# Kernel tuning notes

Hardware: AMD Instinct MI355X
Metric: run time of the kernel (lower is better)

The kernel has to match this reference:

```python
import jax, jax.numpy as jnp
import numpy as np

# Quantization constants from the original module
X_ZP = -66   # int8 zero point
Y_ZP = 160   # uint8 zero point


def setup_inputs() -> dict:
    key = jax.random.key(0)
    k1, k2 = jax.random.split(key)
    # x: [7, B, M, K] int8 in [-128, 127]
    x = jax.random.randint(k1, (7, 8, 512, 1024), -128, 128, dtype=jnp.int32).astype(jnp.int8)
    # y: [B, K, N] uint8 in [0, 255]
    y = jax.random.randint(k2, (8, 1024, 512), 0, 256, dtype=jnp.int32).astype(jnp.uint8)
    return {
        "x": x,
        "y": y,
        "x_scale": jnp.float32(0.03),
        "y_scale": jnp.float32(0.025),
    }


def reference(x, y, x_scale, y_scale):
    # dequantize_per_tensor: (q - zero_point) * scale
    xf = (x.astype(jnp.float32) - jnp.float32(X_ZP)) * x_scale   # [7, B, M, K]
    yf = (y.astype(jnp.float32) - jnp.float32(Y_ZP)) * y_scale   # [B, K, N]
    # torch.matmul broadcast: [7,B,M,K] @ [B,K,N] -> [7,B,M,N]
    return jnp.einsum('gbmk,bkn->gbmn', xf, yf)
```

## Files before the change

kernel.cpp:

```cpp
#include <hip/hip_runtime.h>
#include <stdint.h>

#define AS1 __attribute__((address_space(1)))
#define AS3 __attribute__((address_space(3)))

typedef int v4i __attribute__((ext_vector_type(4)));

constexpr int G = 7, B = 8, M = 512, N = 512, K = 1024;
constexpr int GBn = G * B;

constexpr size_t YT_BYTES = (size_t)B * N * K;
constexpr size_t CSP_CNT  = (size_t)16 * B * N;
constexpr size_t WS_NEEDED = YT_BYTES + CSP_CNT * 4;

__global__ __launch_bounds__(256) void transpose_pack_y(const int* __restrict__ y,
                                                        signed char* __restrict__ yt,
                                                        int* __restrict__ csp) {
    __shared__ unsigned char tile[64][80];
    int n0  = blockIdx.x * 64;
    int k0t = blockIdx.y;
    int k0  = k0t * 64;
    int b   = blockIdx.z;
    int t   = threadIdx.x;

    int r  = t >> 2;
    int c0 = (t & 3) * 16;
    const int* src = y + ((size_t)b * K + k0 + r) * N + n0 + c0;
    uint32_t p[4];
#pragma unroll
    for (int q = 0; q < 4; ++q) {
        int4 v = ((const int4*)src)[q];
        p[q] =  (uint32_t)((v.x & 255) ^ 128)
             | ((uint32_t)((v.y & 255) ^ 128) << 8)
             | ((uint32_t)((v.z & 255) ^ 128) << 16)
             | ((uint32_t)((v.w & 255) ^ 128) << 24);
    }
    *(uint4*)&tile[r][c0] = make_uint4(p[0], p[1], p[2], p[3]);
    __syncthreads();

    int nl = t >> 2;
    int kc = (t & 3) * 16;
    uint32_t q[4];
    int s = 0;
#pragma unroll
    for (int w = 0; w < 4; ++w) {
        uint32_t b0 = tile[kc + w * 4 + 0][nl];
        uint32_t b1 = tile[kc + w * 4 + 1][nl];
        uint32_t b2 = tile[kc + w * 4 + 2][nl];
        uint32_t b3 = tile[kc + w * 4 + 3][nl];
        s += (int)(signed char)b0 + (int)(signed char)b1
           + (int)(signed char)b2 + (int)(signed char)b3;
        q[w] = b0 | (b1 << 8) | (b2 << 16) | (b3 << 24);
    }
    *(uint4*)(yt + ((size_t)b * N + n0 + nl) * K + k0 + kc) = make_uint4(q[0], q[1], q[2], q[3]);

    s += __shfl_xor(s, 1, 64);
    s += __shfl_xor(s, 2, 64);
    if ((t & 3) == 0) csp[(size_t)k0t * (B * N) + b * N + n0 + nl] = s;
}

__global__ __launch_bounds__(512, 4) void gemm_fused(const int* __restrict__ x,
                                                     const signed char* __restrict__ yt,
                                                     const int* __restrict__ csp,
                                                     const float* __restrict__ xsp,
                                                     const float* __restrict__ ysp,
                                                     float* __restrict__ out) {
    __shared__ __align__(16) signed char As[2][128 * 64];
    __shared__ __align__(16) signed char Bs[2][256 * 64];
    __shared__ int cs_lds[256];
    __shared__ int rs_lds[128];

    int id   = blockIdx.x;
    int swz  = (id & 7) * 56 + (id >> 3);
    int gb   = swz >> 3;
    int tile = swz & 7;
    int mt   = tile >> 1;
    int nt   = tile & 1;
    int b    = gb & 7;

    int tid = threadIdx.x, wave = tid >> 6, lane = tid & 63;

    if (tid < 256) {
        int s = 0;
        const int* p = csp + b * N + nt * 256 + tid;
#pragma unroll
        for (int kt = 0; kt < 16; ++kt) s += p[(size_t)kt * (B * N)];
        cs_lds[tid] = s;
    }

    int arow = tid >> 2;
    int akq  = tid & 3;
    const int4* Asrc = (const int4*)(x + ((size_t)(gb * M + mt * 128 + arow)) * K) + akq * 4;
    int aoff = arow * 64 + ((akq ^ ((arow >> 1) & 3)) << 4);

    int brl    = lane >> 2;
    int bchunk = (lane & 3) ^ ((lane >> 3) & 3);
    const signed char* Bsrc = yt + ((size_t)(b * N + nt * 256)) * K;

    int fr = lane & 15;
    int fk = ((lane >> 4) ^ ((fr >> 1) & 3)) << 4;
    int wm = (wave >> 2) * 64;
    int wn = (wave & 3) * 64;

    v4i zero = {0, 0, 0, 0};
    v4i acc[4][4];
#pragma unroll
    for (int i = 0; i < 4; ++i)
#pragma unroll
        for (int j = 0; j < 4; ++j) acc[i][j] = zero;

    int rsum = 0;

    int4 av[4];
#pragma unroll
    for (int q = 0; q < 4; ++q) av[q] = Asrc[q];
#pragma unroll
    for (int c = 0; c < 2; ++c) {
        __builtin_amdgcn_global_load_lds(
            (const AS1 uint32_t*)(Bsrc + (size_t)(wave * 32 + c * 16 + brl) * K + bchunk * 16),
            (AS3 uint32_t*)(&Bs[0][(wave * 32 + c * 16) * 64]), 16, 0, 0);
    }

#pragma unroll 2
    for (int t = 0; t < 16; ++t) {
        int cur = t & 1;

        uint32_t pw[4];
        int s = 0;
#pragma unroll
        for (int q = 0; q < 4; ++q) {
            int4 v = av[q];
            s += v.x + v.y + v.z + v.w;
            pw[q] =  (uint32_t)(v.x & 255)
                 | ((uint32_t)(v.y & 255) << 8)
                 | ((uint32_t)(v.z & 255) << 16)
                 | ((uint32_t)(v.w & 255) << 24);
        }
        rsum += s;
        *(uint4*)(&As[cur][aoff]) = make_uint4(pw[0], pw[1], pw[2], pw[3]);

        __syncthreads();

        if (t < 15) {
#pragma unroll
            for (int q = 0; q < 4; ++q) av[q] = Asrc[(t + 1) * 16 + q];
#pragma unroll
            for (int c = 0; c < 2; ++c) {
                __builtin_amdgcn_global_load_lds(
                    (const AS1 uint32_t*)(Bsrc + (size_t)(wave * 32 + c * 16 + brl) * K
                                          + (t + 1) * 64 + bchunk * 16),
                    (AS3 uint32_t*)(&Bs[cur ^ 1][(wave * 32 + c * 16) * 64]), 16, 0, 0);
            }
        }

        v4i af[4], bf[4];
#pragma unroll
        for (int i = 0; i < 4; ++i)
            af[i] = *(const v4i*)(&As[cur][(wm + i * 16 + fr) * 64 + fk]);
#pragma unroll
        for (int j = 0; j < 4; ++j)
            bf[j] = *(const v4i*)(&Bs[cur][(wn + j * 16 + fr) * 64 + fk]);

#pragma unroll
        for (int i = 0; i < 4; ++i)
#pragma unroll
            for (int j = 0; j < 4; ++j)
                acc[i][j] = __builtin_amdgcn_mfma_i32_16x16x64_i8(af[i], bf[j], acc[i][j], 0, 0, 0);
    }

    rsum += __shfl_xor(rsum, 1, 64);
    rsum += __shfl_xor(rsum, 2, 64);
    if ((tid & 3) == 0) rs_lds[arow] = rsum;
    __syncthreads();

    float sc = xsp[0] * ysp[0];
    int colL = lane & 15;
    int rowQ = (lane >> 4) * 4;
    float* outg = out + (size_t)gb * (M * N) + (size_t)(mt * 128) * N + nt * 256;
#pragma unroll
    for (int i = 0; i < 4; ++i) {
#pragma unroll
        for (int r = 0; r < 4; ++r) {
            int row_l = wm + i * 16 + rowQ + r;
            int rsv = rs_lds[row_l];
#pragma unroll
            for (int j = 0; j < 4; ++j) {
                int col = wn + j * 16 + colL;
                int tv = acc[i][j][r] - 32 * rsv + 66 * cs_lds[col] - 2162688;
                outg[(size_t)row_l * N + col] = sc * (float)tv;
            }
        }
    }
}

__global__ __launch_bounds__(256) void naive_kernel(const int* __restrict__ x,
                                                    const int* __restrict__ y,
                                                    const float* __restrict__ xsp,
                                                    const float* __restrict__ ysp,
                                                    float* __restrict__ out) {
    size_t idx = (size_t)blockIdx.x * 256 + threadIdx.x;
    int n  = (int)(idx & 511);
    int m  = (int)((idx >> 9) & 511);
    int gb = (int)(idx >> 18);
    int b  = gb & 7;
    const int* xr = x + ((size_t)gb * M + m) * K;
    const int* yc = y + (size_t)b * K * N + n;
    int dot = 0, sx = 0, sy = 0;
    for (int k = 0; k < K; ++k) {
        int a = xr[k];
        int c = yc[(size_t)k * N];
        dot += a * c; sx += a; sy += c;
    }
    float s = xsp[0] * ysp[0];
    out[idx] = s * (float)(dot - 160 * sx + 66 * sy - 10813440);
}

extern "C" void kernel_launch(void* const* d_in, const int* in_sizes, int n_in,
                              void* d_out, int out_size, void* d_ws, size_t ws_size,
                              hipStream_t stream) {
    const int*   x  = (const int*)d_in[0];
    const int*   y  = (const int*)d_in[1];
    const float* xs = (const float*)d_in[2];
    const float* ys = (const float*)d_in[3];
    float* out = (float*)d_out;

    if (ws_size < WS_NEEDED) {
        naive_kernel<<<(14680064 + 255) / 256, 256, 0, stream>>>(x, y, xs, ys, out);
        return;
    }

    char* ws = (char*)d_ws;
    signed char* yt  = (signed char*)ws;
    int*         csp = (int*)(ws + YT_BYTES);

    transpose_pack_y<<<dim3(N / 64, K / 64, B), 256, 0, stream>>>(y, yt, csp);
    gemm_fused<<<dim3(448), 512, 0, stream>>>(x, yt, csp, xs, ys, out);
}
```

Before: 250.7 us.

## Widen GEMM tile to full N with 1024-thread blocks

Each block now covers a 128x512 output tile with 16 waves instead of 128x256 with 8 waves. The int32 A tile is loaded, packed and row-summed once per M-tile instead of twice, which halves global reads of x. The cost is twice the LDS for B, larger 1024-thread blocks, and half as many blocks (224), which can hurt occupancy and load balance across CUs.

New measurement: 217.7 us. 13.2% less time.

```diff
diff --git a/kernel.cpp b/kernel.cpp
--- a/kernel.cpp
+++ b/kernel.cpp
@@ -59,48 +59,46 @@
     if ((t & 3) == 0) csp[(size_t)k0t * (B * N) + b * N + n0 + nl] = s;
 }
 
-__global__ __launch_bounds__(512, 4) void gemm_fused(const int* __restrict__ x,
-                                                     const signed char* __restrict__ yt,
-                                                     const int* __restrict__ csp,
-                                                     const float* __restrict__ xsp,
-                                                     const float* __restrict__ ysp,
-                                                     float* __restrict__ out) {
+__global__ __launch_bounds__(1024, 4) void gemm_fused(const int* __restrict__ x,
+                                                      const signed char* __restrict__ yt,
+                                                      const int* __restrict__ csp,
+                                                      const float* __restrict__ xsp,
+                                                      const float* __restrict__ ysp,
+                                                      float* __restrict__ out) {
     __shared__ __align__(16) signed char As[2][128 * 64];
-    __shared__ __align__(16) signed char Bs[2][256 * 64];
-    __shared__ int cs_lds[256];
+    __shared__ __align__(16) signed char Bs[2][512 * 64];
+    __shared__ int cs_lds[512];
     __shared__ int rs_lds[128];
 
-    int id   = blockIdx.x;
-    int swz  = (id & 7) * 56 + (id >> 3);
-    int gb   = swz >> 3;
-    int tile = swz & 7;
-    int mt   = tile >> 1;
-    int nt   = tile & 1;
-    int b    = gb & 7;
+    int id  = blockIdx.x;
+    int swz = (id & 7) * 28 + (id >> 3);
+    int gb  = swz >> 2;
+    int mt  = swz & 3;
+    int b   = gb & 7;
 
     int tid = threadIdx.x, wave = tid >> 6, lane = tid & 63;
 
-    if (tid < 256) {
+    if (tid < 512) {
         int s = 0;
-        const int* p = csp + b * N + nt * 256 + tid;
+        const int* p = csp + b * N + tid;
 #pragma unroll
         for (int kt = 0; kt < 16; ++kt) s += p[(size_t)kt * (B * N)];
         cs_lds[tid] = s;
     }
 
-    int arow = tid >> 2;
-    int akq  = tid & 3;
-    const int4* Asrc = (const int4*)(x + ((size_t)(gb * M + mt * 128 + arow)) * K) + akq * 4;
-    int aoff = arow * 64 + ((akq ^ ((arow >> 1) & 3)) << 4);
+    int arow = tid >> 3;
+    int a8   = tid & 7;
+    const int4* Asrc = (const int4*)(x + ((size_t)(gb * M + mt * 128 + arow)) * K) + a8 * 2;
+    int aoff = arow * 64 + ((((a8 >> 1) ^ ((arow >> 1) & 3))) << 4) + ((a8 & 1) << 3);
 
     int brl    = lane >> 2;
     int bchunk = (lane & 3) ^ ((lane >> 3) & 3);
-    const signed char* Bsrc = yt + ((size_t)(b * N + nt * 256)) * K;
+    const signed char* Bsrc = yt + ((size_t)(b * N)) * K;
 
     int fr = lane & 15;
     int fk = ((lane >> 4) ^ ((fr >> 1) & 3)) << 4;
-    int wm = (wave >> 2) * 64;
-    int wn = (wave & 3) * 64;
+    int wm = (wave >> 3) * 64;
+    int wn = (wave & 7) * 64;
 
     v4i zero = {0, 0, 0, 0};
     v4i acc[4][4];
@@ -111,9 +109,7 @@
 
     int rsum = 0;
 
-    int4 av[4];
-#pragma unroll
-    for (int q = 0; q < 4; ++q) av[q] = Asrc[q];
+    int4 av0 = Asrc[0], av1 = Asrc[1];
 #pragma unroll
     for (int c = 0; c < 2; ++c) {
         __builtin_amdgcn_global_load_lds(
@@ -125,25 +121,25 @@
     for (int t = 0; t < 16; ++t) {
         int cur = t & 1;
 
-        uint32_t pw[4];
-        int s = 0;
-#pragma unroll
-        for (int q = 0; q < 4; ++q) {
-            int4 v = av[q];
-            s += v.x + v.y + v.z + v.w;
-            pw[q] =  (uint32_t)(v.x & 255)
-                 | ((uint32_t)(v.y & 255) << 8)
-                 | ((uint32_t)(v.z & 255) << 16)
-                 | ((uint32_t)(v.w & 255) << 24);
+        {
+            int4 v0 = av0, v1 = av1;
+            rsum += v0.x + v0.y + v0.z + v0.w + v1.x + v1.y + v1.z + v1.w;
+            uint32_t lo =  (uint32_t)(v0.x & 255)
+                        | ((uint32_t)(v0.y & 255) << 8)
+                        | ((uint32_t)(v0.z & 255) << 16)
+                        | ((uint32_t)(v0.w & 255) << 24);
+            uint32_t hi =  (uint32_t)(v1.x & 255)
+                        | ((uint32_t)(v1.y & 255) << 8)
+                        | ((uint32_t)(v1.z & 255) << 16)
+                        | ((uint32_t)(v1.w & 255) << 24);
+            *(uint2*)(&As[cur][aoff]) = make_uint2(lo, hi);
         }
-        rsum += s;
-        *(uint4*)(&As[cur][aoff]) = make_uint4(pw[0], pw[1], pw[2], pw[3]);
 
         __syncthreads();
 
         if (t < 15) {
-#pragma unroll
-            for (int q = 0; q < 4; ++q) av[q] = Asrc[(t + 1) * 16 + q];
+            av0 = Asrc[(t + 1) * 16 + 0];
+            av1 = Asrc[(t + 1) * 16 + 1];
 #pragma unroll
             for (int c = 0; c < 2; ++c) {
                 __builtin_amdgcn_global_load_lds(
@@ -170,13 +166,14 @@
 
     rsum += __shfl_xor(rsum, 1, 64);
     rsum += __shfl_xor(rsum, 2, 64);
-    if ((tid & 3) == 0) rs_lds[arow] = rsum;
+    rsum += __shfl_xor(rsum, 4, 64);
+    if ((tid & 7) == 0) rs_lds[arow] = rsum;
     __syncthreads();
 
     float sc = xsp[0] * ysp[0];
     int colL = lane & 15;
     int rowQ = (lane >> 4) * 4;
-    float* outg = out + (size_t)gb * (M * N) + (size_t)(mt * 128) * N + nt * 256;
+    float* outg = out + (size_t)gb * (M * N) + (size_t)(mt * 128) * N;
 #pragma unroll
     for (int i = 0; i < 4; ++i) {
 #pragma unroll
@@ -234,5 +231,5 @@
     int*         csp = (int*)(ws + YT_BYTES);
 
     transpose_pack_y<<<dim3(N / 64, K / 64, B), 256, 0, stream>>>(y, yt, csp);
-    gemm_fused<<<dim3(448), 512, 0, stream>>>(x, yt, csp, xs, ys, out);
-}
+    gemm_fused<<<dim3(224), 1024, 0, stream>>>(x, yt, csp, xs, ys, out);
+}
```
